# Performance work log

Hardware: AMD Instinct MI355X
Metric: run time of the kernel (lower is better)

Reference implementation:

```python
import jax, jax.numpy as jnp
import numpy as np

HIDDEN = 2048
N_HEADS = 8
N_KV_HEADS = 1
HEAD_DIM = 256
ROPE_THETA = 10000.0
B, S = 2, 2048


def setup_inputs() -> dict:
    key = jax.random.key(0)
    ks = jax.random.split(key, 6)
    sc = 0.02
    hidden_states = jax.random.normal(ks[0], (B, S, HIDDEN), dtype=jnp.float32)
    position_ids = jnp.broadcast_to(jnp.arange(S, dtype=jnp.int64 if jax.config.jax_enable_x64 else jnp.int32), (B, S))
    # additive causal mask: 0 on/below diagonal, large negative above
    causal = jnp.tril(jnp.ones((S, S), dtype=bool))
    attention_mask = jnp.where(causal, 0.0, -1e9).astype(jnp.float32)[None, None, :, :]
    attention_mask = jnp.broadcast_to(attention_mask, (B, 1, S, S))
    Wq = jax.random.normal(ks[1], (HIDDEN, N_HEADS * HEAD_DIM), dtype=jnp.float32) * sc
    Wk = jax.random.normal(ks[2], (HIDDEN, N_KV_HEADS * HEAD_DIM), dtype=jnp.float32) * sc
    Wv = jax.random.normal(ks[3], (HIDDEN, N_KV_HEADS * HEAD_DIM), dtype=jnp.float32) * sc
    Wo = jax.random.normal(ks[4], (N_HEADS * HEAD_DIM, HIDDEN), dtype=jnp.float32) * sc
    return {"hidden_states": hidden_states, "position_ids": position_ids,
            "attention_mask": attention_mask, "Wq": Wq, "Wk": Wk, "Wv": Wv, "Wo": Wo}


def _rotate_half(x):
    x1, x2 = jnp.split(x, 2, axis=-1)
    return jnp.concatenate([-x2, x1], axis=-1)


def _rope_cos_sin(position_ids, dtype):
    # inv_freq: [head_dim/2]
    inv_freq = 1.0 / (ROPE_THETA ** (jnp.arange(0, HEAD_DIM, 2, dtype=jnp.float32) / HEAD_DIM))
    # freqs: [B, S, head_dim/2]
    freqs = position_ids.astype(jnp.float32)[:, :, None] * inv_freq[None, None, :]
    emb = jnp.concatenate([freqs, freqs], axis=-1)  # [B, S, head_dim]
    return jnp.cos(emb).astype(dtype), jnp.sin(emb).astype(dtype)


def reference(hidden_states, position_ids, attention_mask, Wq, Wk, Wv, Wo):
    b, s, _ = hidden_states.shape
    # projections (bias=False)
    q = (hidden_states @ Wq).reshape(b, s, N_HEADS, HEAD_DIM).transpose(0, 2, 1, 3)      # [B,H,S,D]
    k = (hidden_states @ Wk).reshape(b, s, N_KV_HEADS, HEAD_DIM).transpose(0, 2, 1, 3)   # [B,Hk,S,D]
    v = (hidden_states @ Wv).reshape(b, s, N_KV_HEADS, HEAD_DIM).transpose(0, 2, 1, 3)
    cos, sin = _rope_cos_sin(position_ids, hidden_states.dtype)  # [B,S,D]
    cos, sin = cos[:, None], sin[:, None]  # [B,1,S,D]
    q = q * cos + _rotate_half(q) * sin
    k = k * cos + _rotate_half(k) * sin
    # repeat_kv for GQA
    n_rep = N_HEADS // N_KV_HEADS
    k = jnp.repeat(k, n_rep, axis=1)  # [B,H,S,D]
    v = jnp.repeat(v, n_rep, axis=1)
    scale = HEAD_DIM ** -0.5
    scores = jnp.einsum('bhqd,bhkd->bhqk', q, k) * scale + attention_mask
    attn_weights = jax.nn.softmax(scores.astype(jnp.float32), axis=-1).astype(q.dtype)
    attn_out = jnp.einsum('bhqk,bhkd->bhqd', attn_weights, v)
    attn_out = attn_out.transpose(0, 2, 1, 3).reshape(b, s, N_HEADS * HEAD_DIM)
    out = attn_out @ Wo
    return out, attn_weights
```

## Files before the change

### kernel.cpp

```cpp
#include <hip/hip_runtime.h>
#include <hip/hip_bf16.h>
#include <math.h>

typedef __attribute__((ext_vector_type(4))) float f32x4;
typedef __attribute__((ext_vector_type(8))) __bf16 bf16x8;
typedef __attribute__((ext_vector_type(8))) unsigned short u16x8;

#define HID    2048
#define NHEADS 8
#define HDIM   256
#define SEQ    2048
#define BATCH  2
#define ROWS   (BATCH*SEQ)
#define QKVN   (NHEADS*HDIM + 2*HDIM)
#define NBH    (BATCH*NHEADS)

typedef __attribute__((address_space(1))) const void gvoid_t;
typedef __attribute__((address_space(3))) void lvoid_t;

__device__ __forceinline__ void gload16(const void* g, void* l){
  __builtin_amdgcn_global_load_lds((gvoid_t*)g, (lvoid_t*)l, 16, 0, 0);
}

__device__ __forceinline__ float bf2f(unsigned short u){
  union { unsigned int i; float f; } x; x.i = ((unsigned int)u) << 16; return x.f;
}
__device__ __forceinline__ unsigned short f2bf(float f){
  union { float f; unsigned int i; } x; x.f = f;
  unsigned int u = x.i;
  return (unsigned short)((u + 0x7FFFu + ((u >> 16) & 1u)) >> 16);
}

__global__ __launch_bounds__(256)
void k_f32_to_bf16(const float* __restrict__ src, unsigned short* __restrict__ dst){
  long i = ((long)blockIdx.x * 256 + threadIdx.x) * 16;
  f32x4 x0 = *(const f32x4*)(src + i);
  f32x4 x1 = *(const f32x4*)(src + i + 4);
  f32x4 x2 = *(const f32x4*)(src + i + 8);
  f32x4 x3 = *(const f32x4*)(src + i + 12);
  u16x8 w0, w1;
  #pragma unroll
  for (int j = 0; j < 4; ++j){
    w0[j]   = f2bf(x0[j]);
    w0[4+j] = f2bf(x1[j]);
    w1[j]   = f2bf(x2[j]);
    w1[4+j] = f2bf(x3[j]);
  }
  *(u16x8*)(dst + i)     = w0;
  *(u16x8*)(dst + i + 8) = w1;
}

__global__ __launch_bounds__(256)
void k_transpose(const float* __restrict__ src, unsigned short* __restrict__ dst,
                 int srcCols, int dstLd){
  __shared__ float t[32][33];
  int bx = blockIdx.x * 32;
  int by = blockIdx.y * 32;
  int tx = threadIdx.x & 31, ty = threadIdx.x >> 5;
  #pragma unroll
  for (int i = 0; i < 4; ++i){
    int rr = ty + i*8;
    t[rr][tx] = src[(long)(by + rr)*srcCols + bx + tx];
  }
  __syncthreads();
  #pragma unroll
  for (int i = 0; i < 4; ++i){
    int rr = ty + i*8;
    dst[(long)(bx + rr)*dstLd + by + tx] = f2bf(t[tx][rr]);
  }
}

__global__ __launch_bounds__(256)
void k_rope(const unsigned short* __restrict__ qkv, const int* __restrict__ pos_ids,
            unsigned short* __restrict__ Qb, unsigned short* __restrict__ Kb){
  int row = blockIdx.x;
  float pos = (float)pos_ids[row];
  int tid = threadIdx.x;
  const unsigned short* r = qkv + (long)row * QKVN;

  #pragma unroll
  for (int it = 0; it < 4; ++it){
    int p = it*256 + tid;
    int d = p & 127, h = p >> 7;
    int col = h*HDIM + d;
    float inv = (float)exp((double)d * -0.07195578415606393);
    float ang = pos * inv;
    float sn, cs; sincosf(ang, &sn, &cs);
    float x0 = bf2f(r[col]), x1 = bf2f(r[col + 128]);
    Qb[(long)row*HID + col]       = f2bf(x0*cs - x1*sn);
    Qb[(long)row*HID + col + 128] = f2bf(x1*cs + x0*sn);
  }
  if (tid < 128){
    int d = tid;
    float inv = (float)exp((double)d * -0.07195578415606393);
    float ang = pos * inv;
    float sn, cs; sincosf(ang, &sn, &cs);
    float x0 = bf2f(r[HID + d]), x1 = bf2f(r[HID + d + 128]);
    Kb[(long)row*HDIM + d]       = f2bf(x0*cs - x1*sn);
    Kb[(long)row*HDIM + d + 128] = f2bf(x1*cs + x0*sn);
  }
}

__global__ __launch_bounds__(256)
void k_vt(const unsigned short* __restrict__ qkvb, unsigned short* __restrict__ VT){
  __shared__ unsigned short t[32][34];
  int d0 = blockIdx.x * 32, s0 = blockIdx.y * 32, b = blockIdx.z;
  int tx = threadIdx.x & 31, ty = threadIdx.x >> 5;
  #pragma unroll
  for (int i = 0; i < 4; ++i){
    int rr = ty + i*8;
    t[rr][tx] = qkvb[(long)(b*SEQ + s0 + rr)*QKVN + HID + HDIM + d0 + tx];
  }
  __syncthreads();
  #pragma unroll
  for (int i = 0; i < 4; ++i){
    int dd = ty + i*8;
    VT[((long)b*HDIM + d0 + dd)*SEQ + s0 + tx] = t[tx][dd];
  }
}

__global__ __launch_bounds__(512, 4)
void k_fused(const unsigned short* __restrict__ Qb, const unsigned short* __restrict__ Kb,
             const unsigned short* __restrict__ VT, float* __restrict__ S,
             unsigned short* __restrict__ AOb){
  int bh = blockIdx.x, b = bh >> 3, h = bh & 7;
  int ss = 31 - (int)blockIdx.y;
  int qbase = ss * 64;
  int T = ss + 1;

  float* Sh = S + (long)bh * SEQ * SEQ;
  const unsigned short* Qh = Qb + (long)b*SEQ*HID + (long)h*HDIM;
  const unsigned short* Kh = Kb + (long)b*SEQ*HDIM;
  const unsigned short* Vh = VT + (long)b*HDIM*SEQ;

  __shared__ unsigned short lQ[64*256];
  __shared__ unsigned short lK[64*256];
  __shared__ unsigned short lA[64*64];
  __shared__ float lWl[8][64];
  __shared__ float mli[64];

  int tid = threadIdx.x, lane = tid & 63, w = tid >> 6;
  int wr = w >> 2, wc = w & 3;

#define STG(dst_, src_, ld_, rowoff_)                                          \
  { _Pragma("unroll")                                                          \
    for (int t = 0; t < 4; ++t){                                               \
      int seg = w*4 + t;                                                       \
      int row = seg*2 + (lane >> 5);                                           \
      int cb  = ((lane & 31)*16) ^ ((row & 7) << 4);                           \
      gload16((src_) + (long)((rowoff_) + row)*(ld_) + (cb >> 1),              \
              (char*)(dst_) + seg*1024);                                       \
    } }

#define QKT                                                                    \
  { _Pragma("unroll")                                                          \
    for (int kk = 0; kk < 8; ++kk){                                            \
      int rk = wc*16 + (lane & 15);                                            \
      bf16x8 bk = *(const bf16x8*)((const char*)lK + rk*512 +                  \
                   ((kk*64 + (lane >> 4)*16) ^ ((rk & 7) << 4)));              \
      _Pragma("unroll")                                                        \
      for (int m = 0; m < 2; ++m){                                             \
        int rq = wr*32 + m*16 + (lane & 15);                                   \
        bf16x8 aq = *(const bf16x8*)((const char*)lQ + rq*512 +                \
                     ((kk*64 + (lane >> 4)*16) ^ ((rq & 7) << 4)));            \
        acc_s[m] = __builtin_amdgcn_mfma_f32_16x16x32_bf16(aq, bk, acc_s[m], 0, 0, 0); \
      } } }

  f32x4 acc_s[2];
  f32x4 acc_o[4][2];
  float oL[2][4];
  #pragma unroll
  for (int m = 0; m < 2; ++m){
    #pragma unroll
    for (int q = 0; q < 4; ++q){ acc_s[m][q] = 0.f; oL[m][q] = 0.f; }
  }
  #pragma unroll
  for (int m = 0; m < 4; ++m)
    #pragma unroll
    for (int n = 0; n < 2; ++n)
      #pragma unroll
      for (int q = 0; q < 4; ++q) acc_o[m][n][q] = 0.f;

  STG(lQ, Qh, HID, qbase)
  STG(lK, Kh, HDIM, 0)
  for (int kt = 0; kt < T; ++kt){
    asm volatile("s_waitcnt vmcnt(0)" ::: "memory");
    __builtin_amdgcn_s_barrier();
    __builtin_amdgcn_s_setprio(1);
    QKT
    __builtin_amdgcn_s_setprio(0);
    bf16x8 vf[2][2];
    #pragma unroll
    for (int n = 0; n < 2; ++n)
      #pragma unroll
      for (int k2 = 0; k2 < 2; ++k2)
        vf[n][k2] = *(const bf16x8*)(Vh + (long)(w*32 + n*16 + (lane & 15))*SEQ
                                      + kt*64 + k2*32 + (lane >> 4)*8);
    #pragma unroll
    for (int m = 0; m < 2; ++m){
      #pragma unroll
      for (int ri = 0; ri < 4; ++ri){
        int rowl = wr*32 + m*16 + (lane >> 4)*4 + ri;
        int col  = kt*64 + wc*16 + (lane & 15);
        float e = (col <= qbase + rowl) ? __expf(acc_s[m][ri]*0.0625f - 8.0f) : 0.f;
        oL[m][ri] += e;
        *(unsigned short*)((char*)lA + rowl*128 +
            (((wc*16 + (lane & 15))*2) ^ ((rowl & 7) << 4))) = f2bf(e);
        acc_s[m][ri] = 0.f;
      }
    }
    asm volatile("s_waitcnt lgkmcnt(0)" ::: "memory");
    __builtin_amdgcn_s_barrier();
    if (kt + 1 < T) STG(lK, Kh, HDIM, (kt+1)*64)
    __builtin_amdgcn_s_setprio(1);
    #pragma unroll
    for (int k2 = 0; k2 < 2; ++k2){
      #pragma unroll
      for (int m2 = 0; m2 < 4; ++m2){
        int rq = m2*16 + (lane & 15);
        bf16x8 ap = *(const bf16x8*)((const char*)lA + rq*128 +
                     ((k2*64 + (lane >> 4)*16) ^ ((rq & 7) << 4)));
        acc_o[m2][0] = __builtin_amdgcn_mfma_f32_16x16x32_bf16(ap, vf[0][k2], acc_o[m2][0], 0, 0, 0);
        acc_o[m2][1] = __builtin_amdgcn_mfma_f32_16x16x32_bf16(ap, vf[1][k2], acc_o[m2][1], 0, 0, 0);
      }
    }
    __builtin_amdgcn_s_setprio(0);
  }

  #pragma unroll
  for (int m = 0; m < 2; ++m){
    #pragma unroll
    for (int ri = 0; ri < 4; ++ri){
      float v = oL[m][ri];
      #pragma unroll
      for (int off = 1; off < 16; off <<= 1) v += __shfl_xor(v, off);
      if ((lane & 15) == 0)
        lWl[w][wr*32 + m*16 + (lane >> 4)*4 + ri] = v;
    }
  }
  __syncthreads();
  if (tid < 64){
    int g = (tid >> 5) * 4;
    float l = (lWl[g][tid] + lWl[g+1][tid]) + (lWl[g+2][tid] + lWl[g+3][tid]);
    mli[tid] = 1.0f / l;
  }
  __syncthreads();

  float ils[2][4], ilo[4][4];
  #pragma unroll
  for (int m = 0; m < 2; ++m)
    #pragma unroll
    for (int ri = 0; ri < 4; ++ri)
      ils[m][ri] = mli[wr*32 + m*16 + (lane >> 4)*4 + ri];
  #pragma unroll
  for (int m2 = 0; m2 < 4; ++m2)
    #pragma unroll
    for (int ri = 0; ri < 4; ++ri)
      ilo[m2][ri] = mli[m2*16 + (lane >> 4)*4 + ri];

  #pragma unroll
  for (int m2 = 0; m2 < 4; ++m2){
    #pragma unroll
    for (int ri = 0; ri < 4; ++ri){
      int row = qbase + m2*16 + (lane >> 4)*4 + ri;
      long gr = (long)b*SEQ + row;
      #pragma unroll
      for (int n = 0; n < 2; ++n){
        int col = w*32 + n*16 + (lane & 15);
        AOb[gr*HID + h*HDIM + col] = f2bf(acc_o[m2][n][ri] * ilo[m2][ri]);
      }
    }
  }

  STG(lK, Kh, HDIM, 0)
  for (int kt = 0; kt < T; ++kt){
    if (kt == 0) asm volatile("s_waitcnt vmcnt(0)" ::: "memory");
    else         asm volatile("s_waitcnt vmcnt(2)" ::: "memory");
    __builtin_amdgcn_s_barrier();
    __builtin_amdgcn_s_setprio(1);
    QKT
    __builtin_amdgcn_s_setprio(0);
    #pragma unroll
    for (int m = 0; m < 2; ++m){
      #pragma unroll
      for (int ri = 0; ri < 4; ++ri){
        int rowl = wr*32 + m*16 + (lane >> 4)*4 + ri;
        int col  = kt*64 + wc*16 + (lane & 15);
        float p = (col <= qbase + rowl)
                  ? __expf(acc_s[m][ri]*0.0625f - 8.0f) * ils[m][ri] : 0.f;
        *(unsigned short*)((char*)lA + rowl*128 +
            (((wc*16 + (lane & 15))*2) ^ ((rowl & 7) << 4))) = f2bf(p);
        acc_s[m][ri] = 0.f;
      }
    }
    asm volatile("s_waitcnt lgkmcnt(0)" ::: "memory");
    __builtin_amdgcn_s_barrier();
    if (kt + 1 < T) STG(lK, Kh, HDIM, (kt+1)*64)
    {
      int row = tid >> 3, l8 = tid & 7;
      u16x8 v = *(const u16x8*)((const char*)lA + row*128 +
                   ((l8*16) ^ ((row & 7) << 4)));
      f32x4 lo, hi;
      #pragma unroll
      for (int j = 0; j < 4; ++j){ lo[j] = bf2f(v[j]); hi[j] = bf2f(v[4+j]); }
      float* dst = &Sh[(long)(qbase + row)*SEQ + kt*64 + l8*8];
      *(f32x4*)dst       = lo;
      *(f32x4*)(dst + 4) = hi;
    }
  }

  {
    f32x4 z4; z4[0]=0.f; z4[1]=0.f; z4[2]=0.f; z4[3]=0.f;
    int row = qbase + (tid >> 3);
    for (int c = T*64 + (tid & 7)*4; c < SEQ; c += 32)
      *(f32x4*)&Sh[(long)row*SEQ + c] = z4;
  }
#undef STG
#undef QKT
}

template<int OUTF32>
__global__ __launch_bounds__(512, 1)
void gemm256(const unsigned short* __restrict__ A16, const unsigned short* __restrict__ BT,
             void* __restrict__ Cv, int lda, int ldb, int ldc, int K){
  constexpr int BM = 256, BN = 128, BK = 64;
  int m0 = blockIdx.x * BM, n0 = blockIdx.y * BN;

  __shared__ unsigned short lA[2][BM*BK];
  __shared__ unsigned short lB[2][BN*BK];

  int tid = threadIdx.x, lane = tid & 63, w = tid >> 6;
  int wr = w >> 1, wc = w & 1;
  int srow = lane >> 3;
  int vswz = ((lane & 7) ^ ((lane >> 3) & 7)) * 8;

  f32x4 acc[4][4];
  #pragma unroll
  for (int m = 0; m < 4; ++m)
    #pragma unroll
    for (int n = 0; n < 4; ++n)
      #pragma unroll
      for (int q = 0; q < 4; ++q) acc[m][n][q] = 0.f;

  int NT = K / BK;

#define STAGE256(kt_, buf_)                                                    \
  { int k0_ = (kt_) * BK;                                                      \
    _Pragma("unroll")                                                          \
    for (int t = 0; t < 4; ++t){                                               \
      int seg = w*4 + t;                                                       \
      const unsigned short* src = A16 + (long)(m0 + seg*8 + srow)*lda + k0_ + vswz; \
      gload16(src, (char*)lA[buf_] + seg*1024);                                \
    }                                                                          \
    _Pragma("unroll")                                                          \
    for (int t = 0; t < 2; ++t){                                               \
      int seg = w*2 + t;                                                       \
      const unsigned short* src = BT + (long)(n0 + seg*8 + srow)*ldb + k0_ + vswz; \
      gload16(src, (char*)lB[buf_] + seg*1024);                                \
    } }

  STAGE256(0, 0)
  STAGE256(1, 1)
  int cur = 0;

  for (int kt = 0; kt < NT; ++kt){
    if (kt < NT - 1) asm volatile("s_waitcnt vmcnt(6)" ::: "memory");
    else             asm volatile("s_waitcnt vmcnt(0)" ::: "memory");
    __builtin_amdgcn_s_barrier();

    const char* La = (const char*)lA[cur];
    const char* Lb = (const char*)lB[cur];
    __builtin_amdgcn_s_setprio(1);
    #pragma unroll
    for (int kk = 0; kk < 2; ++kk){
      bf16x8 af[4], bfr[4];
      #pragma unroll
      for (int m = 0; m < 4; ++m){
        int row = wr*64 + m*16 + (lane & 15);
        int kb = (kk*64 + (lane >> 4)*16) ^ ((row & 7) << 4);
        af[m] = *(const bf16x8*)(La + row*128 + kb);
      }
      #pragma unroll
      for (int n = 0; n < 4; ++n){
        int row = wc*64 + n*16 + (lane & 15);
        int kb = (kk*64 + (lane >> 4)*16) ^ ((row & 7) << 4);
        bfr[n] = *(const bf16x8*)(Lb + row*128 + kb);
      }
      #pragma unroll
      for (int m = 0; m < 4; ++m)
        #pragma unroll
        for (int n = 0; n < 4; ++n)
          acc[m][n] = __builtin_amdgcn_mfma_f32_16x16x32_bf16(af[m], bfr[n], acc[m][n], 0, 0, 0);
    }
    __builtin_amdgcn_s_setprio(0);
    __builtin_amdgcn_s_barrier();
    if (kt + 2 < NT) STAGE256(kt + 2, cur)
    cur ^= 1;
  }
#undef STAGE256

  #pragma unroll
  for (int m = 0; m < 4; ++m){
    #pragma unroll
    for (int ri = 0; ri < 4; ++ri){
      int orow = m0 + wr*64 + m*16 + (lane >> 4)*4 + ri;
      #pragma unroll
      for (int n = 0; n < 4; ++n){
        int ocol = n0 + wc*64 + n*16 + (lane & 15);
        float vv = acc[m][n][ri];
        if (OUTF32) ((float*)Cv)[(long)orow*ldc + ocol] = vv;
        else        ((unsigned short*)Cv)[(long)orow*ldc + ocol] = f2bf(vv);
      }
    }
  }
}

extern "C" void kernel_launch(void* const* d_in, const int* in_sizes, int n_in,
                              void* d_out, int out_size, void* d_ws, size_t ws_size,
                              hipStream_t stream){
  const float* hs  = (const float*)d_in[0];
  const int*   pos = (const int*)  d_in[1];
  const float* Wq  = (const float*)d_in[3];
  const float* Wk  = (const float*)d_in[4];
  const float* Wv  = (const float*)d_in[5];
  const float* Wo  = (const float*)d_in[6];

  float* out  = (float*)d_out;
  float* Sbuf = out + (long)ROWS * HID;

  unsigned short* wsp   = (unsigned short*)d_ws;
  unsigned short* hsb   = wsp;
  unsigned short* wqkvT = hsb   + (long)ROWS*HID;
  unsigned short* woT   = wqkvT + (long)QKVN*HID;
  unsigned short* qkvb  = woT   + (long)HID*HID;
  unsigned short* Qb    = qkvb  + (long)ROWS*QKVN;
  unsigned short* Kb    = Qb    + (long)ROWS*HID;
  unsigned short* VT    = Kb    + (long)ROWS*HDIM;
  unsigned short* AOb   = VT    + (long)BATCH*HDIM*SEQ;

  k_f32_to_bf16<<<(ROWS*HID)/(256*16), 256, 0, stream>>>(hs, hsb);
  k_transpose<<<dim3(HID/32,  HID/32), 256, 0, stream>>>(Wq, wqkvT, HID, HID);
  k_transpose<<<dim3(HDIM/32, HID/32), 256, 0, stream>>>(Wk, wqkvT + (long)HID*HID, HDIM, HID);
  k_transpose<<<dim3(HDIM/32, HID/32), 256, 0, stream>>>(Wv, wqkvT + (long)(HID+HDIM)*HID, HDIM, HID);
  k_transpose<<<dim3(HID/32,  HID/32), 256, 0, stream>>>(Wo, woT, HID, HID);

  gemm256<0><<<dim3(ROWS/256, QKVN/128), 512, 0, stream>>>(
      hsb, wqkvT, qkvb, HID, HID, QKVN, HID);

  k_rope<<<ROWS, 256, 0, stream>>>(qkvb, pos, Qb, Kb);
  k_vt<<<dim3(HDIM/32, SEQ/32, BATCH), 256, 0, stream>>>(qkvb, VT);

  k_fused<<<dim3(NBH, 32), 512, 0, stream>>>(Qb, Kb, VT, Sbuf, AOb);

  gemm256<1><<<dim3(ROWS/256, HID/128), 512, 0, stream>>>(
      AOb, woT, out, HID, HID, HID, HID);
}
```

Before: 330.9 us.

## Double-buffer 32-column K tiles in fused attention and re-split waves

The fused attention kernel now walks keys in 32-wide tiles and keeps two K tiles in shared memory, so the next tile is prefetched while the current one is computed. Wave layout changes to 4x2 with one 16x16 score accumulator per wave, and the P tile switches from XOR swizzle to a padded stride. V fragments are loaded per tile ahead of the barrier. RoPE computes inverse frequency with float exp2f instead of double exp. The cost is twice as many loop iterations and barriers and smaller MFMA work per iteration, in exchange for overlapping K loads with compute and lower register pressure.

```diff
diff --git a/kernel.cpp b/kernel.cpp
--- a/kernel.cpp
+++ b/kernel.cpp
@@ -5,6 +5,7 @@
 typedef __attribute__((ext_vector_type(4))) float f32x4;
 typedef __attribute__((ext_vector_type(8))) __bf16 bf16x8;
 typedef __attribute__((ext_vector_type(8))) unsigned short u16x8;
+typedef __attribute__((ext_vector_type(4))) unsigned short u16x4;
 
 #define HID    2048
 #define NHEADS 8
@@ -83,7 +84,7 @@
     int p = it*256 + tid;
     int d = p & 127, h = p >> 7;
     int col = h*HDIM + d;
-    float inv = (float)exp((double)d * -0.07195578415606393);
+    float inv = exp2f((float)d * -0.10381025296523132f);
     float ang = pos * inv;
     float sn, cs; sincosf(ang, &sn, &cs);
     float x0 = bf2f(r[col]), x1 = bf2f(r[col + 128]);
@@ -92,7 +93,7 @@
   }
   if (tid < 128){
     int d = tid;
-    float inv = (float)exp((double)d * -0.07195578415606393);
+    float inv = exp2f((float)d * -0.10381025296523132f);
     float ang = pos * inv;
     float sn, cs; sincosf(ang, &sn, &cs);
     float x0 = bf2f(r[HID + d]), x1 = bf2f(r[HID + d + 128]);
@@ -126,7 +127,7 @@
   int bh = blockIdx.x, b = bh >> 3, h = bh & 7;
   int ss = 31 - (int)blockIdx.y;
   int qbase = ss * 64;
-  int T = ss + 1;
+  int T = 2 * (ss + 1);
 
   float* Sh = S + (long)bh * SEQ * SEQ;
   const unsigned short* Qh = Qb + (long)b*SEQ*HID + (long)h*HDIM;
@@ -134,46 +135,50 @@
   const unsigned short* Vh = VT + (long)b*HDIM*SEQ;
 
   __shared__ unsigned short lQ[64*256];
-  __shared__ unsigned short lK[64*256];
-  __shared__ unsigned short lA[64*64];
+  __shared__ unsigned short lK[2][32*256];
+  __shared__ unsigned short lA[64*40];
   __shared__ float lWl[8][64];
   __shared__ float mli[64];
 
   int tid = threadIdx.x, lane = tid & 63, w = tid >> 6;
-  int wr = w >> 2, wc = w & 3;
-
-#define STG(dst_, src_, ld_, rowoff_)                                          \
-  { _Pragma("unroll")                                                          \
-    for (int t = 0; t < 4; ++t){                                               \
-      int seg = w*4 + t;                                                       \
-      int row = seg*2 + (lane >> 5);                                           \
-      int cb  = ((lane & 31)*16) ^ ((row & 7) << 4);                           \
-      gload16((src_) + (long)((rowoff_) + row)*(ld_) + (cb >> 1),              \
-              (char*)(dst_) + seg*1024);                                       \
+  int wr = w >> 1, wc = w & 1;
+
+#define STAGE_Q                                                                 \
+  { _Pragma("unroll")                                                           \
+    for (int t = 0; t < 4; ++t){                                                \
+      int seg = w*4 + t;                                                        \
+      int row = seg*2 + (lane >> 5);                                            \
+      int cb  = ((lane & 31)*16) ^ ((row & 7) << 4);                            \
+      gload16(Qh + (long)(qbase + row)*HID + (cb >> 1), (char*)lQ + seg*1024);  \
     } }
 
-#define QKT                                                                    \
-  { _Pragma("unroll")                                                          \
-    for (int kk = 0; kk < 8; ++kk){                                            \
-      int rk = wc*16 + (lane & 15);                                            \
-      bf16x8 bk = *(const bf16x8*)((const char*)lK + rk*512 +                  \
-                   ((kk*64 + (lane >> 4)*16) ^ ((rk & 7) << 4)));              \
-      _Pragma("unroll")                                                        \
-      for (int m = 0; m < 2; ++m){                                             \
-        int rq = wr*32 + m*16 + (lane & 15);                                   \
-        bf16x8 aq = *(const bf16x8*)((const char*)lQ + rq*512 +                \
-                     ((kk*64 + (lane >> 4)*16) ^ ((rq & 7) << 4)));            \
-        acc_s[m] = __builtin_amdgcn_mfma_f32_16x16x32_bf16(aq, bk, acc_s[m], 0, 0, 0); \
-      } } }
-
-  f32x4 acc_s[2];
+#define STAGE_K(kt_, buf_)                                                      \
+  { _Pragma("unroll")                                                           \
+    for (int t = 0; t < 2; ++t){                                                \
+      int seg = w*2 + t;                                                        \
+      int row = seg*2 + (lane >> 5);                                            \
+      int cb  = ((lane & 31)*16) ^ ((row & 7) << 4);                            \
+      gload16(Kh + (long)((kt_)*32 + row)*HDIM + (cb >> 1),                     \
+              (char*)lK[buf_] + seg*1024);                                      \
+    } }
+
+#define QKT(buf_)                                                               \
+  { _Pragma("unroll")                                                           \
+    for (int kk = 0; kk < 8; ++kk){                                             \
+      int rk = wc*16 + (lane & 15);                                             \
+      bf16x8 bk = *(const bf16x8*)((const char*)lK[buf_] + rk*512 +             \
+                   ((kk*64 + (lane >> 4)*16) ^ ((rk & 7) << 4)));               \
+      int rq = wr*16 + (lane & 15);                                             \
+      bf16x8 aq = *(const bf16x8*)((const char*)lQ + rq*512 +                   \
+                   ((kk*64 + (lane >> 4)*16) ^ ((rq & 7) << 4)));               \
+      accs = __builtin_amdgcn_mfma_f32_16x16x32_bf16(aq, bk, accs, 0, 0, 0);    \
+    } }
+
+  f32x4 accs;
   f32x4 acc_o[4][2];
-  float oL[2][4];
-  #pragma unroll
-  for (int m = 0; m < 2; ++m){
-    #pragma unroll
-    for (int q = 0; q < 4; ++q){ acc_s[m][q] = 0.f; oL[m][q] = 0.f; }
-  }
+  float oL[4];
+  #pragma unroll
+  for (int q = 0; q < 4; ++q){ accs[q] = 0.f; oL[q] = 0.f; }
   #pragma unroll
   for (int m = 0; m < 4; ++m)
     #pragma unroll
@@ -181,77 +186,59 @@
       #pragma unroll
       for (int q = 0; q < 4; ++q) acc_o[m][n][q] = 0.f;
 
-  STG(lQ, Qh, HID, qbase)
-  STG(lK, Kh, HDIM, 0)
+  STAGE_Q
+  STAGE_K(0, 0)
+  STAGE_K(1, 1)
   for (int kt = 0; kt < T; ++kt){
-    asm volatile("s_waitcnt vmcnt(0)" ::: "memory");
+    bf16x8 vf0 = *(const bf16x8*)(Vh + (long)(w*32 +      (lane & 15))*SEQ + kt*32 + (lane >> 4)*8);
+    bf16x8 vf1 = *(const bf16x8*)(Vh + (long)(w*32 + 16 + (lane & 15))*SEQ + kt*32 + (lane >> 4)*8);
+    asm volatile("s_waitcnt vmcnt(4)" ::: "memory");
     __builtin_amdgcn_s_barrier();
     __builtin_amdgcn_s_setprio(1);
-    QKT
+    QKT(kt & 1)
     __builtin_amdgcn_s_setprio(0);
-    bf16x8 vf[2][2];
-    #pragma unroll
-    for (int n = 0; n < 2; ++n)
-      #pragma unroll
-      for (int k2 = 0; k2 < 2; ++k2)
-        vf[n][k2] = *(const bf16x8*)(Vh + (long)(w*32 + n*16 + (lane & 15))*SEQ
-                                      + kt*64 + k2*32 + (lane >> 4)*8);
-    #pragma unroll
-    for (int m = 0; m < 2; ++m){
-      #pragma unroll
-      for (int ri = 0; ri < 4; ++ri){
-        int rowl = wr*32 + m*16 + (lane >> 4)*4 + ri;
-        int col  = kt*64 + wc*16 + (lane & 15);
-        float e = (col <= qbase + rowl) ? __expf(acc_s[m][ri]*0.0625f - 8.0f) : 0.f;
-        oL[m][ri] += e;
-        *(unsigned short*)((char*)lA + rowl*128 +
-            (((wc*16 + (lane & 15))*2) ^ ((rowl & 7) << 4))) = f2bf(e);
-        acc_s[m][ri] = 0.f;
-      }
+    #pragma unroll
+    for (int ri = 0; ri < 4; ++ri){
+      int rowl = wr*16 + (lane >> 4)*4 + ri;
+      int coll = wc*16 + (lane & 15);
+      float e = (kt*32 + coll <= qbase + rowl) ? __expf(accs[ri]*0.0625f - 8.0f) : 0.f;
+      oL[ri] += e;
+      lA[rowl*40 + coll] = f2bf(e);
+      accs[ri] = 0.f;
     }
     asm volatile("s_waitcnt lgkmcnt(0)" ::: "memory");
     __builtin_amdgcn_s_barrier();
-    if (kt + 1 < T) STG(lK, Kh, HDIM, (kt+1)*64)
+    if (kt + 2 < T) STAGE_K(kt + 2, kt & 1)
     __builtin_amdgcn_s_setprio(1);
     #pragma unroll
-    for (int k2 = 0; k2 < 2; ++k2){
-      #pragma unroll
-      for (int m2 = 0; m2 < 4; ++m2){
-        int rq = m2*16 + (lane & 15);
-        bf16x8 ap = *(const bf16x8*)((const char*)lA + rq*128 +
-                     ((k2*64 + (lane >> 4)*16) ^ ((rq & 7) << 4)));
-        acc_o[m2][0] = __builtin_amdgcn_mfma_f32_16x16x32_bf16(ap, vf[0][k2], acc_o[m2][0], 0, 0, 0);
-        acc_o[m2][1] = __builtin_amdgcn_mfma_f32_16x16x32_bf16(ap, vf[1][k2], acc_o[m2][1], 0, 0, 0);
-      }
+    for (int m2 = 0; m2 < 4; ++m2){
+      int rq = m2*16 + (lane & 15);
+      bf16x8 ap = *(const bf16x8*)&lA[rq*40 + (lane >> 4)*8];
+      acc_o[m2][0] = __builtin_amdgcn_mfma_f32_16x16x32_bf16(ap, vf0, acc_o[m2][0], 0, 0, 0);
+      acc_o[m2][1] = __builtin_amdgcn_mfma_f32_16x16x32_bf16(ap, vf1, acc_o[m2][1], 0, 0, 0);
     }
     __builtin_amdgcn_s_setprio(0);
   }
 
   #pragma unroll
-  for (int m = 0; m < 2; ++m){
-    #pragma unroll
-    for (int ri = 0; ri < 4; ++ri){
-      float v = oL[m][ri];
-      #pragma unroll
-      for (int off = 1; off < 16; off <<= 1) v += __shfl_xor(v, off);
-      if ((lane & 15) == 0)
-        lWl[w][wr*32 + m*16 + (lane >> 4)*4 + ri] = v;
-    }
+  for (int ri = 0; ri < 4; ++ri){
+    float v = oL[ri];
+    #pragma unroll
+    for (int off = 1; off < 16; off <<= 1) v += __shfl_xor(v, off);
+    if ((lane & 15) == 0)
+      lWl[w][wr*16 + (lane >> 4)*4 + ri] = v;
   }
   __syncthreads();
   if (tid < 64){
-    int g = (tid >> 5) * 4;
-    float l = (lWl[g][tid] + lWl[g+1][tid]) + (lWl[g+2][tid] + lWl[g+3][tid]);
-    mli[tid] = 1.0f / l;
+    int g = (tid >> 4) * 2;
+    mli[tid] = 1.0f / (lWl[g][tid] + lWl[g+1][tid]);
   }
   __syncthreads();
 
-  float ils[2][4], ilo[4][4];
-  #pragma unroll
-  for (int m = 0; m < 2; ++m)
-    #pragma unroll
-    for (int ri = 0; ri < 4; ++ri)
-      ils[m][ri] = mli[wr*32 + m*16 + (lane >> 4)*4 + ri];
+  float ils[4], ilo[4][4];
+  #pragma unroll
+  for (int ri = 0; ri < 4; ++ri)
+    ils[ri] = mli[wr*16 + (lane >> 4)*4 + ri];
   #pragma unroll
   for (int m2 = 0; m2 < 4; ++m2)
     #pragma unroll
@@ -272,50 +259,46 @@
     }
   }
 
-  STG(lK, Kh, HDIM, 0)
+  STAGE_K(0, 0)
+  STAGE_K(1, 1)
   for (int kt = 0; kt < T; ++kt){
-    if (kt == 0) asm volatile("s_waitcnt vmcnt(0)" ::: "memory");
-    else         asm volatile("s_waitcnt vmcnt(2)" ::: "memory");
+    if (kt == 0)           asm volatile("s_waitcnt vmcnt(2)" ::: "memory");
+    else if (kt + 1 >= T)  asm volatile("s_waitcnt vmcnt(1)" ::: "memory");
+    else                   asm volatile("s_waitcnt vmcnt(4)" ::: "memory");
     __builtin_amdgcn_s_barrier();
     __builtin_amdgcn_s_setprio(1);
-    QKT
+    QKT(kt & 1)
     __builtin_amdgcn_s_setprio(0);
     #pragma unroll
-    for (int m = 0; m < 2; ++m){
-      #pragma unroll
-      for (int ri = 0; ri < 4; ++ri){
-        int rowl = wr*32 + m*16 + (lane >> 4)*4 + ri;
-        int col  = kt*64 + wc*16 + (lane & 15);
-        float p = (col <= qbase + rowl)
-                  ? __expf(acc_s[m][ri]*0.0625f - 8.0f) * ils[m][ri] : 0.f;
-        *(unsigned short*)((char*)lA + rowl*128 +
-            (((wc*16 + (lane & 15))*2) ^ ((rowl & 7) << 4))) = f2bf(p);
-        acc_s[m][ri] = 0.f;
-      }
+    for (int ri = 0; ri < 4; ++ri){
+      int rowl = wr*16 + (lane >> 4)*4 + ri;
+      int coll = wc*16 + (lane & 15);
+      float p = (kt*32 + coll <= qbase + rowl)
+                ? __expf(accs[ri]*0.0625f - 8.0f) * ils[ri] : 0.f;
+      lA[rowl*40 + coll] = f2bf(p);
+      accs[ri] = 0.f;
     }
     asm volatile("s_waitcnt lgkmcnt(0)" ::: "memory");
     __builtin_amdgcn_s_barrier();
-    if (kt + 1 < T) STG(lK, Kh, HDIM, (kt+1)*64)
+    if (kt + 2 < T) STAGE_K(kt + 2, kt & 1)
     {
       int row = tid >> 3, l8 = tid & 7;
-      u16x8 v = *(const u16x8*)((const char*)lA + row*128 +
-                   ((l8*16) ^ ((row & 7) << 4)));
-      f32x4 lo, hi;
-      #pragma unroll
-      for (int j = 0; j < 4; ++j){ lo[j] = bf2f(v[j]); hi[j] = bf2f(v[4+j]); }
-      float* dst = &Sh[(long)(qbase + row)*SEQ + kt*64 + l8*8];
-      *(f32x4*)dst       = lo;
-      *(f32x4*)(dst + 4) = hi;
+      u16x4 v = *(const u16x4*)&lA[row*40 + l8*4];
+      f32x4 o;
+      #pragma unroll
+      for (int j = 0; j < 4; ++j) o[j] = bf2f(v[j]);
+      *(f32x4*)&Sh[(long)(qbase + row)*SEQ + kt*32 + l8*4] = o;
     }
   }
 
   {
     f32x4 z4; z4[0]=0.f; z4[1]=0.f; z4[2]=0.f; z4[3]=0.f;
     int row = qbase + (tid >> 3);
-    for (int c = T*64 + (tid & 7)*4; c < SEQ; c += 32)
+    for (int c = T*32 + (tid & 7)*4; c < SEQ; c += 32)
       *(f32x4*)&Sh[(long)row*SEQ + c] = z4;
   }
-#undef STG
+#undef STAGE_Q
+#undef STAGE_K
 #undef QKT
 }
 
```

New measurement: 342.3 us. 3.5% more time.
